# Kernel optimization log

Measured on AMD Instinct MI355X. Metric: run time of the kernel, lower is better.

The kernel has to match this reference:

```python
import jax, jax.numpy as jnp
import numpy as np

NUM_HEADS = 16
NUM_KV_HEADS = 4
HEAD_DIM = 64
HIDDEN = 1024
BATCH, SEQ = 2, 2048
CAUSAL = False


def _rotate_half(x):
    x1, x2 = jnp.split(x, 2, axis=-1)
    return jnp.concatenate([-x2, x1], axis=-1)


def setup_inputs() -> dict:
    key = jax.random.key(0)
    k1, k2, k3 = jax.random.split(key, 3)
    hidden_states = jax.random.normal(k1, (BATCH, SEQ, HIDDEN), dtype=jnp.float32)
    # realistic rotary tables
    inv_freq = 1.0 / (10000.0 ** (np.arange(0, HEAD_DIM, 2, dtype=np.float32) / HEAD_DIM))
    t = np.arange(SEQ, dtype=np.float32)
    freqs = np.outer(t, inv_freq)                      # [S, D/2]
    emb = np.concatenate([freqs, freqs], axis=-1)      # [S, D]
    cos = jnp.asarray(np.cos(emb), dtype=jnp.float32)
    sin = jnp.asarray(np.sin(emb), dtype=jnp.float32)
    qkv_out = (NUM_HEADS + 2 * NUM_KV_HEADS) * HEAD_DIM
    w_qkv = jax.random.normal(k2, (qkv_out, HIDDEN), dtype=jnp.float32) * (HIDDEN ** -0.5)
    w_o = jax.random.normal(k3, (HIDDEN, NUM_HEADS * HEAD_DIM), dtype=jnp.float32) * ((NUM_HEADS * HEAD_DIM) ** -0.5)
    return {"hidden_states": hidden_states, "cos": cos, "sin": sin, "w_qkv": w_qkv, "w_o": w_o}


def reference(hidden_states, cos, sin, w_qkv, w_o):
    b, s, _ = hidden_states.shape
    qkv = jnp.einsum('bsh,oh->bso', hidden_states, w_qkv)
    qkv = qkv.reshape(b, s, NUM_HEADS + 2 * NUM_KV_HEADS, HEAD_DIM)
    q = qkv[:, :, :NUM_HEADS]                                    # [b,s,Hq,d]
    k = qkv[:, :, NUM_HEADS:NUM_HEADS + NUM_KV_HEADS]            # [b,s,Hkv,d]
    v = qkv[:, :, NUM_HEADS + NUM_KV_HEADS:]                     # [b,s,Hkv,d]
    # RoPE (HF style): broadcast cos/sin [s,d] over batch and heads
    c = cos[None, :, None, :]
    sn = sin[None, :, None, :]
    q = q * c + _rotate_half(q) * sn
    k = k * c + _rotate_half(k) * sn
    # GQA: repeat kv heads to match q heads
    rep = NUM_HEADS // NUM_KV_HEADS
    k = jnp.repeat(k, rep, axis=2)
    v = jnp.repeat(v, rep, axis=2)
    scale = HEAD_DIM ** -0.5
    scores = jnp.einsum('bqhd,bkhd->bhqk', q, k) * scale
    if CAUSAL:
        mask = jnp.tril(jnp.ones((s, s), dtype=bool))
        scores = jnp.where(mask[None, None], scores, jnp.finfo(scores.dtype).min)
    probs = jax.nn.softmax(scores, axis=-1)
    attn = jnp.einsum('bhqk,bkhd->bqhd', probs, v)
    attn = attn.reshape(b, s, NUM_HEADS * HEAD_DIM)
    return jnp.einsum('bso,ho->bsh', attn, w_o)
```

## Files before the change

kernel.cpp:

```cpp
#include <hip/hip_runtime.h>
#include <hip/hip_bf16.h>

typedef unsigned short u16;
typedef unsigned int u32;
typedef __attribute__((ext_vector_type(8))) short short8;
typedef __attribute__((ext_vector_type(4))) float f32x4;
typedef __attribute__((ext_vector_type(16))) float f32x16;
typedef __attribute__((ext_vector_type(4))) u32 u32x4;

__device__ __forceinline__ u16 f2b(float f) {
    __hip_bfloat16 h = __float2bfloat16(f);
    return *reinterpret_cast<u16*>(&h);
}
__device__ __forceinline__ float b2f(u16 u) {
    __hip_bfloat16 h;
    *reinterpret_cast<u16*>(&h) = u;
    return __bfloat162float(h);
}
__device__ __forceinline__ u32 cvtpk(float lo, float hi_) {
    u32 r;
    asm("v_cvt_pk_bf16_f32 %0, %1, %2" : "=v"(r) : "v"(lo), "v"(hi_));
    return r;
}
__device__ __forceinline__ float fexp2(float x) {
    float r;
    asm("v_exp_f32 %0, %1" : "=v"(r) : "v"(x));
    return r;
}
__device__ __forceinline__ void gload16(const void* g, void* l) {
    __builtin_amdgcn_global_load_lds(
        (const __attribute__((address_space(1))) unsigned int*)g,
        (__attribute__((address_space(3))) unsigned int*)l, 16, 0, 0);
}

__global__ void convert_kernel(const float* __restrict__ X, const float* __restrict__ W1,
                               const float* __restrict__ W2,
                               u16* __restrict__ Xb, u16* __restrict__ W1b, u16* __restrict__ W2b) {
    int idx = blockIdx.x * 256 + threadIdx.x;
    const float* src; u16* dst; int off;
    if (idx < 1048576)        { src = X;  dst = Xb;  off = idx; }
    else if (idx < 1441792)   { src = W1; dst = W1b; off = idx - 1048576; }
    else                      { src = W2; dst = W2b; off = idx - 1441792; }
    float4 v = reinterpret_cast<const float4*>(src)[off];
    ushort4 o;
    o.x = f2b(v.x); o.y = f2b(v.y); o.z = f2b(v.z); o.w = f2b(v.w);
    reinterpret_cast<ushort4*>(dst)[off] = o;
}

template <typename OUT>
__global__ __launch_bounds__(256) void gemm_bt(const u16* __restrict__ A, const u16* __restrict__ B,
                                               OUT* __restrict__ C, int M, int N, int K) {
    __shared__ u16 As[2][64 * 32];
    __shared__ u16 Bs[2][128 * 32];
    const int tid = threadIdx.x;
    const int lane = tid & 63, wave = tid >> 6;
    const int wm = wave >> 1, wn = wave & 1;
    const int row16 = lane & 15, kgrp = lane >> 4;
    const int bm = blockIdx.x, bn = blockIdx.y;
    const int nk = K >> 5;
    const u16* Abase = A + (size_t)bm * 64 * K;
    const u16* Bbase = B + (size_t)bn * 128 * K;

    f32x4 acc[2][4];
#pragma unroll
    for (int i = 0; i < 2; ++i)
#pragma unroll
        for (int j = 0; j < 4; ++j) acc[i][j] = {0.f, 0.f, 0.f, 0.f};

    auto stage = [&](int buf, int kt) {
        {
            int row = tid >> 2, c = tid & 3;
            int cs = c ^ ((row >> 1) & 3);
            gload16(Abase + (size_t)row * K + kt * 32 + cs * 8, &As[buf][tid * 8]);
        }
#pragma unroll
        for (int it = 0; it < 2; ++it) {
            int chunk = it * 256 + tid;
            int row = chunk >> 2, c = chunk & 3;
            int cs = c ^ ((row >> 1) & 3);
            gload16(Bbase + (size_t)row * K + kt * 32 + cs * 8, &Bs[buf][chunk * 8]);
        }
    };

    stage(0, 0);
    __syncthreads();
    for (int kt = 0; kt < nk; ++kt) {
        int cur = kt & 1;
        if (kt + 1 < nk) stage(cur ^ 1, kt + 1);
        short8 af[2], bfr[4];
#pragma unroll
        for (int mf = 0; mf < 2; ++mf) {
            int r = wm * 32 + mf * 16 + row16;
            af[mf] = *(const short8*)&As[cur][r * 32 + (kgrp ^ ((r >> 1) & 3)) * 8];
        }
#pragma unroll
        for (int nf = 0; nf < 4; ++nf) {
            int r = wn * 64 + nf * 16 + row16;
            bfr[nf] = *(const short8*)&Bs[cur][r * 32 + (kgrp ^ ((r >> 1) & 3)) * 8];
        }
#pragma unroll
        for (int mf = 0; mf < 2; ++mf)
#pragma unroll
            for (int nf = 0; nf < 4; ++nf)
                acc[mf][nf] = __builtin_amdgcn_mfma_f32_16x16x32_bf16(af[mf], bfr[nf], acc[mf][nf], 0, 0, 0);
        __syncthreads();
    }
#pragma unroll
    for (int mf = 0; mf < 2; ++mf)
#pragma unroll
        for (int r = 0; r < 4; ++r) {
            int row = bm * 64 + wm * 32 + mf * 16 + kgrp * 4 + r;
#pragma unroll
            for (int nf = 0; nf < 4; ++nf) {
                int col = bn * 128 + wn * 64 + nf * 16 + row16;
                float v = acc[mf][nf][r];
                if constexpr (sizeof(OUT) == 2) C[(size_t)row * N + col] = f2b(v);
                else                            C[(size_t)row * N + col] = v;
            }
        }
}

__global__ void rope_kernel(const u16* __restrict__ qkv, const float* __restrict__ cosb,
                            const float* __restrict__ sinb, u16* __restrict__ Qa,
                            u16* __restrict__ Ka) {
    int idx = blockIdx.x * 256 + threadIdx.x;
    if (idx < 2097152) {
        int d = idx & 31, h = (idx >> 5) & 15, m = idx >> 9;
        int s = m & 2047, b = m >> 11;
        const u16* src = qkv + (size_t)m * 1536 + h * 64 + d;
        float q1 = b2f(src[0]), q2 = b2f(src[32]);
        float c = cosb[s * 64 + d], sn = sinb[s * 64 + d];
        u16* dst = Qa + ((size_t)(b * 16 + h) * 2048 + s) * 64 + d;
        dst[0]  = f2b((q1 * c - q2 * sn) * 0.18033688f);
        dst[32] = f2b((q2 * c + q1 * sn) * 0.18033688f);
    } else {
        int t = idx - 2097152;
        int d = t & 31, kh = (t >> 5) & 3, m = t >> 7;
        int s = m & 2047, b = m >> 11;
        const u16* src = qkv + (size_t)m * 1536 + (16 + kh) * 64 + d;
        float q1 = b2f(src[0]), q2 = b2f(src[32]);
        float c = cosb[s * 64 + d], sn = sinb[s * 64 + d];
        u16* dst = Ka + ((size_t)(b * 4 + kh) * 2048 + s) * 64 + d;
        dst[0]  = f2b(q1 * c - q2 * sn);
        dst[32] = f2b(q2 * c + q1 * sn);
    }
}

__global__ __launch_bounds__(256) void vtrans_kernel(const u16* __restrict__ qkv, u16* __restrict__ Vt) {
    __shared__ u16 T[64 * 71];
    const int tid = threadIdx.x;
    const int sblk = blockIdx.x, kh = blockIdx.y, b = blockIdx.z;
    const u16* src = qkv + (size_t)(b * 2048 + sblk * 64) * 1536 + 1280 + kh * 64;
#pragma unroll
    for (int it = 0; it < 2; ++it) {
        int u = it * 256 + tid;
        int s = u >> 3, c = u & 7;
        short8 v = *(const short8*)(src + (size_t)s * 1536 + c * 8);
#pragma unroll
        for (int i = 0; i < 8; ++i)
            T[(c * 8 + i) * 71 + s] = (u16)v[i];
    }
    __syncthreads();
    u16* dst = Vt + (size_t)(b * 4 + kh) * 64 * 2048 + sblk * 64;
#pragma unroll
    for (int it = 0; it < 2; ++it) {
        int u = it * 256 + tid;
        int d = u >> 3, s0 = (u & 7) * 8;
        short8 o;
#pragma unroll
        for (int i = 0; i < 8; ++i) o[i] = (short)T[d * 71 + s0 + i];
        *(short8*)(dst + (size_t)d * 2048 + s0) = o;
    }
}

__global__ __launch_bounds__(256) void attn_kernel(const u16* __restrict__ Qa,
                                                   const u16* __restrict__ Ka,
                                                   const u16* __restrict__ Vt,
                                                   u16* __restrict__ Ob) {
    __shared__ u16 Ks[2][64 * 64];
    __shared__ u16 Vs[2][64 * 64];
    const int tid = threadIdx.x, lane = tid & 63, wave = tid >> 6;
    const int q32 = lane & 31, hi = lane >> 5;
    const int qt = blockIdx.x, h = blockIdx.y, b = blockIdx.z;
    const int kh = h >> 2;
    const u16* Qp = Qa + ((size_t)(b * 16 + h) * 2048 + qt * 128 + wave * 32) * 64;
    const u16* Kp = Ka + (size_t)(b * 4 + kh) * 2048 * 64;
    const u16* Vp = Vt + (size_t)(b * 4 + kh) * 64 * 2048;

    short8 qf[4];
#pragma unroll
    for (int dt = 0; dt < 4; ++dt)
        qf[dt] = *(const short8*)(Qp + q32 * 64 + dt * 16 + hi * 8);

    f32x16 oacc[2];
#pragma unroll
    for (int i = 0; i < 2; ++i)
#pragma unroll
        for (int r = 0; r < 16; ++r) oacc[i][r] = 0.f;
    float lpx = 0.f, lpy = 0.f;

    auto stageKV = [&](int buf, int kvt) {
#pragma unroll
        for (int it = 0; it < 2; ++it) {
            int chunk = it * 256 + tid;
            int row = chunk >> 3, c = chunk & 7;
            gload16(Kp + (size_t)(kvt * 64 + row) * 64 + ((c ^ (row & 7)) * 8), &Ks[buf][chunk * 8]);
        }
#pragma unroll
        for (int it = 0; it < 2; ++it) {
            int chunk = it * 256 + tid;
            int row = chunk >> 3, c = chunk & 7;
            gload16(Vp + (size_t)row * 2048 + kvt * 64 + ((c ^ (row & 7)) * 8), &Vs[buf][chunk * 8]);
        }
    };

    stageKV(0, 0);
    __syncthreads();
    for (int kvt = 0; kvt < 32; ++kvt) {
        const int cur = kvt & 1;
        if (kvt + 1 < 32) stageKV(cur ^ 1, kvt + 1);

        f32x16 S[2];
#pragma unroll
        for (int i = 0; i < 2; ++i)
#pragma unroll
            for (int r = 0; r < 16; ++r) S[i][r] = 0.f;
        __builtin_amdgcn_s_setprio(1);
#pragma unroll
        for (int kt2 = 0; kt2 < 2; ++kt2) {
            int krow = kt2 * 32 + q32;
#pragma unroll
            for (int dt = 0; dt < 4; ++dt) {
                short8 kf = *(const short8*)&Ks[cur][(krow * 8 + ((dt * 2 + hi) ^ (krow & 7))) * 8];
                S[kt2] = __builtin_amdgcn_mfma_f32_32x32x16_bf16(kf, qf[dt], S[kt2], 0, 0, 0);
            }
        }
        __builtin_amdgcn_s_setprio(0);

#pragma unroll
        for (int kt2 = 0; kt2 < 2; ++kt2)
#pragma unroll
            for (int r = 0; r < 16; r += 2) {
                float p0 = fexp2(S[kt2][r]);
                float p1 = fexp2(S[kt2][r + 1]);
                S[kt2][r] = p0; S[kt2][r + 1] = p1;
                lpx += p0; lpy += p1;
            }

        __builtin_amdgcn_s_setprio(1);
#pragma unroll
        for (int kc = 0; kc < 4; ++kc) {
            const int kt2 = kc >> 1, R = (kc & 1) * 8;
            u32 a0 = cvtpk(S[kt2][R + 0], S[kt2][R + 1]);
            u32 b0 = cvtpk(S[kt2][R + 4], S[kt2][R + 5]);
            asm("v_permlane32_swap_b32 %0, %1" : "+v"(a0), "+v"(b0));
            u32 a1 = cvtpk(S[kt2][R + 2], S[kt2][R + 3]);
            u32 b1 = cvtpk(S[kt2][R + 6], S[kt2][R + 7]);
            asm("v_permlane32_swap_b32 %0, %1" : "+v"(a1), "+v"(b1));
            u32x4 pw; pw[0] = a0; pw[1] = a1; pw[2] = b0; pw[3] = b1;
            short8 pf = __builtin_bit_cast(short8, pw);
#pragma unroll
            for (int dt2 = 0; dt2 < 2; ++dt2) {
                int vrow = dt2 * 32 + q32;
                short8 vf = *(const short8*)&Vs[cur][(vrow * 8 + ((kc * 2 + hi) ^ (vrow & 7))) * 8];
                oacc[dt2] = __builtin_amdgcn_mfma_f32_32x32x16_bf16(vf, pf, oacc[dt2], 0, 0, 0);
            }
        }
        __builtin_amdgcn_s_setprio(0);
        __syncthreads();
    }

    float lpart = lpx + lpy;
    float l = lpart + __shfl_xor(lpart, 32);
    float inv = 1.f / l;
    const size_t mbase = ((size_t)(b * 2048 + qt * 128 + wave * 32 + q32)) * 1024 + h * 64;
#pragma unroll
    for (int dt2 = 0; dt2 < 2; ++dt2)
#pragma unroll
        for (int rq = 0; rq < 4; ++rq) {
            ushort4 o;
            o.x = f2b(oacc[dt2][rq * 4 + 0] * inv);
            o.y = f2b(oacc[dt2][rq * 4 + 1] * inv);
            o.z = f2b(oacc[dt2][rq * 4 + 2] * inv);
            o.w = f2b(oacc[dt2][rq * 4 + 3] * inv);
            *(ushort4*)&Ob[mbase + dt2 * 32 + rq * 8 + hi * 4] = o;
        }
}

extern "C" void kernel_launch(void* const* d_in, const int* in_sizes, int n_in,
                              void* d_out, int out_size, void* d_ws, size_t ws_size,
                              hipStream_t stream) {
    const float* X    = (const float*)d_in[0];
    const float* cosb = (const float*)d_in[1];
    const float* sinb = (const float*)d_in[2];
    const float* Wqkv = (const float*)d_in[3];
    const float* Wo   = (const float*)d_in[4];
    float* out = (float*)d_out;
    char* ws = (char*)d_ws;

    u16* Xbf    = (u16*)(ws);
    u16* Wqkvbf = (u16*)(ws + 8388608);
    u16* Wobf   = (u16*)(ws + 11534336);
    u16* QKV    = (u16*)(ws + 13631488);
    u16* Qa     = (u16*)(ws + 26214400);
    u16* Ka     = (u16*)(ws + 34603008);
    u16* Vt     = (u16*)(ws + 36700160);
    u16* attnb  = Xbf;

    convert_kernel<<<6656, 256, 0, stream>>>(X, Wqkv, Wo, Xbf, Wqkvbf, Wobf);
    gemm_bt<u16><<<dim3(64, 12), 256, 0, stream>>>(Xbf, Wqkvbf, QKV, 4096, 1536, 1024);
    rope_kernel<<<10240, 256, 0, stream>>>(QKV, cosb, sinb, Qa, Ka);
    vtrans_kernel<<<dim3(32, 4, 2), 256, 0, stream>>>(QKV, Vt);
    attn_kernel<<<dim3(16, 16, 2), 256, 0, stream>>>(Qa, Ka, Vt, attnb);
    gemm_bt<float><<<dim3(64, 8), 256, 0, stream>>>(attnb, Wobf, out, 4096, 1024, 1024);
}
```

Measured before the change: 179.7 us.

## Split attention KV range across blocks and deepen GEMM K tile to 64

The attention kernel now splits the 2048-key range into two halves across extra blocks, writing unnormalized bf16 partial outputs and row sums. A new combine kernel adds the two halves and normalizes. Separately, the GEMM stages K in 64-wide tiles with an 8-way XOR swizzle, issues twice the MFMAs per barrier, and raises wave priority around the MFMA loop. The aim is more blocks for attention (512 to 1024) and fewer barriers in the GEMMs. The cost is an extra launch, more memory traffic, and an extra bf16 rounding of the partials. The split appears to rely on a fixed softmax offset rather than a running max, so the halves can be added directly.

New measurement: 180.3 us. No clear change (+0.4%).

```diff
diff --git a/kernel.cpp b/kernel.cpp
--- a/kernel.cpp
+++ b/kernel.cpp
@@ -50,14 +50,14 @@
 template <typename OUT>
 __global__ __launch_bounds__(256) void gemm_bt(const u16* __restrict__ A, const u16* __restrict__ B,
                                                OUT* __restrict__ C, int M, int N, int K) {
-    __shared__ u16 As[2][64 * 32];
-    __shared__ u16 Bs[2][128 * 32];
+    __shared__ u16 As[2][64 * 64];
+    __shared__ u16 Bs[2][128 * 64];
     const int tid = threadIdx.x;
     const int lane = tid & 63, wave = tid >> 6;
     const int wm = wave >> 1, wn = wave & 1;
     const int row16 = lane & 15, kgrp = lane >> 4;
     const int bm = blockIdx.x, bn = blockIdx.y;
-    const int nk = K >> 5;
+    const int nk = K >> 6;
     const u16* Abase = A + (size_t)bm * 64 * K;
     const u16* Bbase = B + (size_t)bn * 128 * K;
 
@@ -68,17 +68,19 @@
         for (int j = 0; j < 4; ++j) acc[i][j] = {0.f, 0.f, 0.f, 0.f};
 
     auto stage = [&](int buf, int kt) {
-        {
-            int row = tid >> 2, c = tid & 3;
-            int cs = c ^ ((row >> 1) & 3);
-            gload16(Abase + (size_t)row * K + kt * 32 + cs * 8, &As[buf][tid * 8]);
-        }
 #pragma unroll
         for (int it = 0; it < 2; ++it) {
             int chunk = it * 256 + tid;
-            int row = chunk >> 2, c = chunk & 3;
-            int cs = c ^ ((row >> 1) & 3);
-            gload16(Bbase + (size_t)row * K + kt * 32 + cs * 8, &Bs[buf][chunk * 8]);
+            int row = chunk >> 3, c = chunk & 7;
+            int cs = c ^ (row & 7);
+            gload16(Abase + (size_t)row * K + kt * 64 + cs * 8, &As[buf][chunk * 8]);
+        }
+#pragma unroll
+        for (int it = 0; it < 4; ++it) {
+            int chunk = it * 256 + tid;
+            int row = chunk >> 3, c = chunk & 7;
+            int cs = c ^ (row & 7);
+            gload16(Bbase + (size_t)row * K + kt * 64 + cs * 8, &Bs[buf][chunk * 8]);
         }
     };
 
@@ -87,22 +89,30 @@
     for (int kt = 0; kt < nk; ++kt) {
         int cur = kt & 1;
         if (kt + 1 < nk) stage(cur ^ 1, kt + 1);
-        short8 af[2], bfr[4];
+        short8 af[2][2], bfr[4][2];
 #pragma unroll
         for (int mf = 0; mf < 2; ++mf) {
             int r = wm * 32 + mf * 16 + row16;
-            af[mf] = *(const short8*)&As[cur][r * 32 + (kgrp ^ ((r >> 1) & 3)) * 8];
+#pragma unroll
+            for (int kk = 0; kk < 2; ++kk)
+                af[mf][kk] = *(const short8*)&As[cur][(r * 8 + ((kk * 4 + kgrp) ^ (r & 7))) * 8];
         }
 #pragma unroll
         for (int nf = 0; nf < 4; ++nf) {
             int r = wn * 64 + nf * 16 + row16;
-            bfr[nf] = *(const short8*)&Bs[cur][r * 32 + (kgrp ^ ((r >> 1) & 3)) * 8];
-        }
-#pragma unroll
-        for (int mf = 0; mf < 2; ++mf)
-#pragma unroll
-            for (int nf = 0; nf < 4; ++nf)
-                acc[mf][nf] = __builtin_amdgcn_mfma_f32_16x16x32_bf16(af[mf], bfr[nf], acc[mf][nf], 0, 0, 0);
+#pragma unroll
+            for (int kk = 0; kk < 2; ++kk)
+                bfr[nf][kk] = *(const short8*)&Bs[cur][(r * 8 + ((kk * 4 + kgrp) ^ (r & 7))) * 8];
+        }
+        __builtin_amdgcn_s_setprio(1);
+#pragma unroll
+        for (int kk = 0; kk < 2; ++kk)
+#pragma unroll
+            for (int mf = 0; mf < 2; ++mf)
+#pragma unroll
+                for (int nf = 0; nf < 4; ++nf)
+                    acc[mf][nf] = __builtin_amdgcn_mfma_f32_16x16x32_bf16(af[mf][kk], bfr[nf][kk], acc[mf][nf], 0, 0, 0);
+        __builtin_amdgcn_s_setprio(0);
         __syncthreads();
     }
 #pragma unroll
@@ -176,12 +186,14 @@
 __global__ __launch_bounds__(256) void attn_kernel(const u16* __restrict__ Qa,
                                                    const u16* __restrict__ Ka,
                                                    const u16* __restrict__ Vt,
-                                                   u16* __restrict__ Ob) {
+                                                   u16* __restrict__ Opart,
+                                                   float* __restrict__ lpart) {
     __shared__ u16 Ks[2][64 * 64];
     __shared__ u16 Vs[2][64 * 64];
     const int tid = threadIdx.x, lane = tid & 63, wave = tid >> 6;
     const int q32 = lane & 31, hi = lane >> 5;
-    const int qt = blockIdx.x, h = blockIdx.y, b = blockIdx.z;
+    const int qt = blockIdx.x, h = blockIdx.y, z = blockIdx.z;
+    const int b = z & 1, kvs = z >> 1;
     const int kh = h >> 2;
     const u16* Qp = Qa + ((size_t)(b * 16 + h) * 2048 + qt * 128 + wave * 32) * 64;
     const u16* Kp = Ka + (size_t)(b * 4 + kh) * 2048 * 64;
@@ -214,17 +226,18 @@
         }
     };
 
-    stageKV(0, 0);
+    const int kv0 = kvs * 16;
+    stageKV(0, kv0);
     __syncthreads();
-    for (int kvt = 0; kvt < 32; ++kvt) {
-        const int cur = kvt & 1;
-        if (kvt + 1 < 32) stageKV(cur ^ 1, kvt + 1);
+    for (int i = 0; i < 16; ++i) {
+        const int cur = i & 1;
+        if (i + 1 < 16) stageKV(cur ^ 1, kv0 + i + 1);
 
         f32x16 S[2];
 #pragma unroll
-        for (int i = 0; i < 2; ++i)
-#pragma unroll
-            for (int r = 0; r < 16; ++r) S[i][r] = 0.f;
+        for (int j = 0; j < 2; ++j)
+#pragma unroll
+            for (int r = 0; r < 16; ++r) S[j][r] = 0.f;
         __builtin_amdgcn_s_setprio(1);
 #pragma unroll
         for (int kt2 = 0; kt2 < 2; ++kt2) {
@@ -270,21 +283,39 @@
         __syncthreads();
     }
 
-    float lpart = lpx + lpy;
-    float l = lpart + __shfl_xor(lpart, 32);
-    float inv = 1.f / l;
-    const size_t mbase = ((size_t)(b * 2048 + qt * 128 + wave * 32 + q32)) * 1024 + h * 64;
+    const int qrow = qt * 128 + wave * 32 + q32;
+    float lp = lpx + lpy;
+    float l = lp + __shfl_xor(lp, 32);
+    if (hi == 0) lpart[((size_t)z * 16 + h) * 2048 + qrow] = l;
+    const size_t pbase = (((size_t)z * 16 + h) * 2048 + qrow) * 64;
 #pragma unroll
     for (int dt2 = 0; dt2 < 2; ++dt2)
 #pragma unroll
         for (int rq = 0; rq < 4; ++rq) {
             ushort4 o;
-            o.x = f2b(oacc[dt2][rq * 4 + 0] * inv);
-            o.y = f2b(oacc[dt2][rq * 4 + 1] * inv);
-            o.z = f2b(oacc[dt2][rq * 4 + 2] * inv);
-            o.w = f2b(oacc[dt2][rq * 4 + 3] * inv);
-            *(ushort4*)&Ob[mbase + dt2 * 32 + rq * 8 + hi * 4] = o;
-        }
+            o.x = f2b(oacc[dt2][rq * 4 + 0]);
+            o.y = f2b(oacc[dt2][rq * 4 + 1]);
+            o.z = f2b(oacc[dt2][rq * 4 + 2]);
+            o.w = f2b(oacc[dt2][rq * 4 + 3]);
+            *(ushort4*)&Opart[pbase + dt2 * 32 + rq * 8 + hi * 4] = o;
+        }
+}
+
+__global__ void combine_kernel(const u16* __restrict__ Opart, const float* __restrict__ lpart,
+                               u16* __restrict__ attnb) {
+    int t = blockIdx.x * 256 + threadIdx.x;
+    int d4 = t & 15, q = (t >> 4) & 2047, h = (t >> 15) & 15, b = t >> 19;
+    size_t i1 = (((size_t)b * 16 + h) * 2048 + q) * 64 + d4 * 4;
+    ushort4 o1 = *(const ushort4*)&Opart[i1];
+    ushort4 o2 = *(const ushort4*)&Opart[i1 + 4194304];
+    size_t li = ((size_t)b * 16 + h) * 2048 + q;
+    float inv = 1.f / (lpart[li] + lpart[li + 65536]);
+    ushort4 o;
+    o.x = f2b((b2f(o1.x) + b2f(o2.x)) * inv);
+    o.y = f2b((b2f(o1.y) + b2f(o2.y)) * inv);
+    o.z = f2b((b2f(o1.z) + b2f(o2.z)) * inv);
+    o.w = f2b((b2f(o1.w) + b2f(o2.w)) * inv);
+    *(ushort4*)&attnb[((size_t)(b * 2048 + q)) * 1024 + h * 64 + d4 * 4] = o;
 }
 
 extern "C" void kernel_launch(void* const* d_in, const int* in_sizes, int n_in,
@@ -306,11 +337,14 @@
     u16* Ka     = (u16*)(ws + 34603008);
     u16* Vt     = (u16*)(ws + 36700160);
     u16* attnb  = Xbf;
+    float* lpart = (float*)QKV;
+    u16* Opart  = (u16*)d_out;
 
     convert_kernel<<<6656, 256, 0, stream>>>(X, Wqkv, Wo, Xbf, Wqkvbf, Wobf);
     gemm_bt<u16><<<dim3(64, 12), 256, 0, stream>>>(Xbf, Wqkvbf, QKV, 4096, 1536, 1024);
     rope_kernel<<<10240, 256, 0, stream>>>(QKV, cosb, sinb, Qa, Ka);
     vtrans_kernel<<<dim3(32, 4, 2), 256, 0, stream>>>(QKV, Vt);
-    attn_kernel<<<dim3(16, 16, 2), 256, 0, stream>>>(Qa, Ka, Vt, attnb);
+    attn_kernel<<<dim3(16, 16, 4), 256, 0, stream>>>(Qa, Ka, Vt, Opart, lpart);
+    combine_kernel<<<4096, 256, 0, stream>>>(Opart, lpart, attnb);
     gemm_bt<float><<<dim3(64, 8), 256, 0, stream>>>(attnb, Wobf, out, 4096, 1024, 1024);
 }
```

## Double GEMM K-tile to 64 and emulate exp2 with polynomial plus ldexp

Applied to the files above, without the earlier changes.

The bf16 GEMM now stages 64-wide K tiles with an 8-way XOR swizzle. That halves the number of barrier iterations, and the MFMA block runs under raised wave priority. In the attention kernel, the hardware v_exp_f32 transcendental is replaced by a cubic polynomial on the fractional part followed by v_ldexp_f32, moving the exponential work from the transcendental unit onto FMA ALUs. The polynomial costs several extra VALU instructions per element and is less accurate, though bf16 rounding of P likely hides the error.

Result: no change. 176.3 us (-1.9%).

```diff
diff --git a/kernel.cpp b/kernel.cpp
--- a/kernel.cpp
+++ b/kernel.cpp
@@ -22,9 +22,15 @@
     asm("v_cvt_pk_bf16_f32 %0, %1, %2" : "=v"(r) : "v"(lo), "v"(hi_));
     return r;
 }
-__device__ __forceinline__ float fexp2(float x) {
+__device__ __forceinline__ float fexp2p(float x) {
+    float nf = __builtin_rintf(x);
+    float f = x - nf;
+    float p = __builtin_fmaf(f, 0.05550411f, 0.24022651f);
+    p = __builtin_fmaf(f, p, 0.69314718f);
+    p = __builtin_fmaf(f, p, 1.0f);
+    int n = (int)nf;
     float r;
-    asm("v_exp_f32 %0, %1" : "=v"(r) : "v"(x));
+    asm("v_ldexp_f32 %0, %1, %2" : "=v"(r) : "v"(p), "v"(n));
     return r;
 }
 __device__ __forceinline__ void gload16(const void* g, void* l) {
@@ -50,14 +56,14 @@
 template <typename OUT>
 __global__ __launch_bounds__(256) void gemm_bt(const u16* __restrict__ A, const u16* __restrict__ B,
                                                OUT* __restrict__ C, int M, int N, int K) {
-    __shared__ u16 As[2][64 * 32];
-    __shared__ u16 Bs[2][128 * 32];
+    __shared__ u16 As[2][64 * 64];
+    __shared__ u16 Bs[2][128 * 64];
     const int tid = threadIdx.x;
     const int lane = tid & 63, wave = tid >> 6;
     const int wm = wave >> 1, wn = wave & 1;
     const int row16 = lane & 15, kgrp = lane >> 4;
     const int bm = blockIdx.x, bn = blockIdx.y;
-    const int nk = K >> 5;
+    const int nk = K >> 6;
     const u16* Abase = A + (size_t)bm * 64 * K;
     const u16* Bbase = B + (size_t)bn * 128 * K;
 
@@ -68,17 +74,19 @@
         for (int j = 0; j < 4; ++j) acc[i][j] = {0.f, 0.f, 0.f, 0.f};
 
     auto stage = [&](int buf, int kt) {
-        {
-            int row = tid >> 2, c = tid & 3;
-            int cs = c ^ ((row >> 1) & 3);
-            gload16(Abase + (size_t)row * K + kt * 32 + cs * 8, &As[buf][tid * 8]);
-        }
 #pragma unroll
         for (int it = 0; it < 2; ++it) {
             int chunk = it * 256 + tid;
-            int row = chunk >> 2, c = chunk & 3;
-            int cs = c ^ ((row >> 1) & 3);
-            gload16(Bbase + (size_t)row * K + kt * 32 + cs * 8, &Bs[buf][chunk * 8]);
+            int row = chunk >> 3, c = chunk & 7;
+            int cs = c ^ (row & 7);
+            gload16(Abase + (size_t)row * K + kt * 64 + cs * 8, &As[buf][chunk * 8]);
+        }
+#pragma unroll
+        for (int it = 0; it < 4; ++it) {
+            int chunk = it * 256 + tid;
+            int row = chunk >> 3, c = chunk & 7;
+            int cs = c ^ (row & 7);
+            gload16(Bbase + (size_t)row * K + kt * 64 + cs * 8, &Bs[buf][chunk * 8]);
         }
     };
 
@@ -87,22 +95,30 @@
     for (int kt = 0; kt < nk; ++kt) {
         int cur = kt & 1;
         if (kt + 1 < nk) stage(cur ^ 1, kt + 1);
-        short8 af[2], bfr[4];
+        short8 af[2][2], bfr[4][2];
 #pragma unroll
         for (int mf = 0; mf < 2; ++mf) {
             int r = wm * 32 + mf * 16 + row16;
-            af[mf] = *(const short8*)&As[cur][r * 32 + (kgrp ^ ((r >> 1) & 3)) * 8];
+#pragma unroll
+            for (int kk = 0; kk < 2; ++kk)
+                af[mf][kk] = *(const short8*)&As[cur][(r * 8 + ((kk * 4 + kgrp) ^ (r & 7))) * 8];
         }
 #pragma unroll
         for (int nf = 0; nf < 4; ++nf) {
             int r = wn * 64 + nf * 16 + row16;
-            bfr[nf] = *(const short8*)&Bs[cur][r * 32 + (kgrp ^ ((r >> 1) & 3)) * 8];
-        }
-#pragma unroll
-        for (int mf = 0; mf < 2; ++mf)
-#pragma unroll
-            for (int nf = 0; nf < 4; ++nf)
-                acc[mf][nf] = __builtin_amdgcn_mfma_f32_16x16x32_bf16(af[mf], bfr[nf], acc[mf][nf], 0, 0, 0);
+#pragma unroll
+            for (int kk = 0; kk < 2; ++kk)
+                bfr[nf][kk] = *(const short8*)&Bs[cur][(r * 8 + ((kk * 4 + kgrp) ^ (r & 7))) * 8];
+        }
+        __builtin_amdgcn_s_setprio(1);
+#pragma unroll
+        for (int kk = 0; kk < 2; ++kk)
+#pragma unroll
+            for (int mf = 0; mf < 2; ++mf)
+#pragma unroll
+                for (int nf = 0; nf < 4; ++nf)
+                    acc[mf][nf] = __builtin_amdgcn_mfma_f32_16x16x32_bf16(af[mf][kk], bfr[nf][kk], acc[mf][nf], 0, 0, 0);
+        __builtin_amdgcn_s_setprio(0);
         __syncthreads();
     }
 #pragma unroll
@@ -222,9 +238,9 @@
 
         f32x16 S[2];
 #pragma unroll
-        for (int i = 0; i < 2; ++i)
-#pragma unroll
-            for (int r = 0; r < 16; ++r) S[i][r] = 0.f;
+        for (int j = 0; j < 2; ++j)
+#pragma unroll
+            for (int r = 0; r < 16; ++r) S[j][r] = 0.f;
         __builtin_amdgcn_s_setprio(1);
 #pragma unroll
         for (int kt2 = 0; kt2 < 2; ++kt2) {
@@ -241,8 +257,8 @@
         for (int kt2 = 0; kt2 < 2; ++kt2)
 #pragma unroll
             for (int r = 0; r < 16; r += 2) {
-                float p0 = fexp2(S[kt2][r]);
-                float p1 = fexp2(S[kt2][r + 1]);
+                float p0 = fexp2p(S[kt2][r]);
+                float p1 = fexp2p(S[kt2][r + 1]);
                 S[kt2][r] = p0; S[kt2][r + 1] = p1;
                 lpx += p0; lpy += p1;
             }
```
